# Optimization experiments

Hardware: AMD Instinct MI355X
Metric: run time of the kernel (lower is better)

Reference implementation:

```python
import jax, jax.numpy as jnp
import numpy as np

X_DIM = 512
Y_DIM = 512
HID = 300
N = 2048


def setup_inputs() -> dict:
    key = jax.random.key(0)
    ks = jax.random.split(key, 8)
    scale = 0.05
    return {
        "pos_local": jax.random.normal(ks[0], (N, X_DIM), jnp.float32),
        "pos_global": jax.random.normal(ks[1], (N, Y_DIM), jnp.float32),
        "neg_local": jax.random.normal(ks[2], (N, X_DIM), jnp.float32),
        "neg_global": jax.random.normal(ks[3], (N, Y_DIM), jnp.float32),
        "W1": jax.random.normal(ks[4], (X_DIM + Y_DIM, HID), jnp.float32) * scale,
        "b1": jnp.zeros((HID,), jnp.float32),
        "W2": jax.random.normal(ks[5], (HID, 1), jnp.float32) * scale,
        "b2": jnp.zeros((1,), jnp.float32),
        "batch_size": 256,
    }


def reference(pos_local, pos_global, neg_local, neg_global, W1, b1, W2, b2, batch_size):
    # Split first-layer weight into local/global halves so we never materialize
    # the concatenated pair tensor: F(cat(l, g)) uses l @ W1l + g @ W1g.
    W1l, W1g = W1[:X_DIM], W1[X_DIM:]
    w2, bias2 = W2[:, 0], b2[0]

    # Positive branch: plain batched MLP, chunking does not change the math.
    h0 = jax.nn.relu(pos_local @ W1l + pos_global @ W1g + b1)  # [N, HID]
    t0 = jax.nn.softplus(h0 @ w2 + bias2).mean()

    # Negative branch: per chunk of size B, pair (local_j, global_i),
    # score[i, j] = F(local_j, global_i); logsumexp over j, mean over i.
    nc = neg_local.shape[0] // batch_size
    nl = neg_local.reshape(nc, batch_size, X_DIM)
    ng = neg_global.reshape(nc, batch_size, Y_DIM)

    def chunk_term(carry, lg):
        l, g = lg                                   # [B, x], [B, y]
        lp = l @ W1l                                # [B, HID]
        gp = g @ W1g                                # [B, HID]
        h = jax.nn.relu(gp[:, None, :] + lp[None, :, :] + b1)  # [B, B, HID]
        s = jax.nn.softplus(h @ w2 + bias2)         # [B, B]
        val = jax.scipy.special.logsumexp(s, axis=1).mean()
        return carry + val, None

    total, _ = jax.lax.scan(chunk_term, jnp.float32(0.0), (nl, ng))
    t1 = total / nc

    lower_bound = t0 - t1
    return -lower_bound
```

## Files before the change

### kernel.cpp

```cpp
#include <hip/hip_runtime.h>
#include <math.h>

#define NR   2048
#define XD   512
#define HID  300
#define BS   256
#define NCH  8
#define NPAD 320
#define KTOT 1024
#define GSTR 304
#define NBLK 544

typedef __attribute__((ext_vector_type(8))) short bf16x8;
typedef __attribute__((ext_vector_type(4))) float f32x4;

__device__ __forceinline__ float softplus_f(float x) {
    return fmaxf(x, 0.f) + log1pf(__expf(-fabsf(x)));
}
__device__ __forceinline__ unsigned short f2bf(float f) {
    unsigned int u = __float_as_uint(f);
    u += 0x7FFFu + ((u >> 16) & 1u);
    return (unsigned short)(u >> 16);
}

__global__ __launch_bounds__(256) void convert(
    const float* __restrict__ pl, const float* __restrict__ pg,
    const float* __restrict__ nl, const float* __restrict__ ng,
    const float* __restrict__ W1,
    unsigned short* __restrict__ Aneg, unsigned short* __restrict__ Apos,
    unsigned short* __restrict__ Wt, unsigned int* __restrict__ counter)
{
    const int b = blockIdx.x, tid = threadIdx.x;
    if (b == 0 && tid == 0) *counter = 0u;
    if (b < 4096) {
        const int m = (b < 2048) ? b : b - 2048;
        const float* lo = (b < 2048) ? nl : pl;
        const float* hi = (b < 2048) ? ng : pg;
        unsigned short* dst = (b < 2048) ? Aneg : Apos;
        const int kq = tid * 4;
        const float4 v = (kq < XD) ? *(const float4*)(lo + m * XD + kq)
                                   : *(const float4*)(hi + m * XD + kq - XD);
        ushort4 o;
        o.x = f2bf(v.x); o.y = f2bf(v.y); o.z = f2bf(v.z); o.w = f2bf(v.w);
        *(ushort4*)(dst + m * KTOT + kq) = o;
    } else {
        __shared__ unsigned short ts[16][72];
        const int t = b - 4096;
        const int nt = t % 20, kt = t / 20;
        const int n = nt * 16 + (tid & 15);
        const int kl = tid >> 4;
        #pragma unroll
        for (int j = 0; j < 4; ++j) {
            const int k = kt * 64 + kl * 4 + j;
            const float val = (n < HID) ? W1[k * HID + n] : 0.f;
            ts[tid & 15][kl * 4 + j] = f2bf(val);
        }
        __syncthreads();
        const int nw = tid >> 4, kw = (tid & 15) * 4;
        ushort4 o;
        o.x = ts[nw][kw]; o.y = ts[nw][kw + 1]; o.z = ts[nw][kw + 2]; o.w = ts[nw][kw + 3];
        *(ushort4*)(Wt + (nt * 16 + nw) * KTOT + kt * 64 + kw) = o;
    }
}

__global__ __launch_bounds__(64) void mfma_gemm(
    const unsigned short* __restrict__ Aneg, const unsigned short* __restrict__ Apos,
    const unsigned short* __restrict__ Wt, const float* __restrict__ b1,
    float* __restrict__ LP4, float* __restrict__ GPB,
    float* __restrict__ P0a, float* __restrict__ P0b)
{
    const int job = blockIdx.z;
    const int m0 = blockIdx.x * 32, n0 = blockIdx.y * 32;
    const int lane = threadIdx.x;
    const int r = lane & 15, g = lane >> 4;

    const unsigned short* A = (job >= 2) ? Apos : Aneg;
    const int kbeg = (job & 1) ? XD : 0;

    const unsigned short* a0p = A  + (m0 + r) * KTOT + kbeg + 8 * g;
    const unsigned short* a1p = a0p + 16 * KTOT;
    const unsigned short* b0p = Wt + (n0 + r) * KTOT + kbeg + 8 * g;
    const unsigned short* b1p = b0p + 16 * KTOT;

    f32x4 acc00 = {0,0,0,0}, acc01 = {0,0,0,0}, acc10 = {0,0,0,0}, acc11 = {0,0,0,0};

    #pragma unroll 8
    for (int k = 0; k < XD; k += 32) {
        const bf16x8 a0 = *(const bf16x8*)(a0p + k);
        const bf16x8 a1 = *(const bf16x8*)(a1p + k);
        const bf16x8 w0 = *(const bf16x8*)(b0p + k);
        const bf16x8 w1 = *(const bf16x8*)(b1p + k);
        acc00 = __builtin_amdgcn_mfma_f32_16x16x32_bf16(a0, w0, acc00, 0, 0, 0);
        acc01 = __builtin_amdgcn_mfma_f32_16x16x32_bf16(a0, w1, acc01, 0, 0, 0);
        acc10 = __builtin_amdgcn_mfma_f32_16x16x32_bf16(a1, w0, acc10, 0, 0, 0);
        acc11 = __builtin_amdgcn_mfma_f32_16x16x32_bf16(a1, w1, acc11, 0, 0, 0);
    }

    f32x4 accs[2][2] = {{acc00, acc01}, {acc10, acc11}};
    #pragma unroll
    for (int mi = 0; mi < 2; ++mi) {
        #pragma unroll
        for (int ni = 0; ni < 2; ++ni) {
            const int n = n0 + ni * 16 + r;
            const int mb = m0 + mi * 16 + 4 * g;
            const f32x4 v = accs[mi][ni];
            if (job == 0) {
                float* base = LP4 + ((size_t)(n >> 2) * NR + mb) * 4 + (n & 3);
                base[0] = v[0]; base[4] = v[1]; base[8] = v[2]; base[12] = v[3];
            } else if (n < HID) {
                const float bias = (job == 1) ? b1[n] : 0.f;
                float* out = (job == 1) ? GPB : ((job == 2) ? P0a : P0b);
                #pragma unroll
                for (int j = 0; j < 4; ++j)
                    out[(size_t)(mb + j) * GSTR + n] = v[j] + bias;
            }
        }
    }
}

__global__ __launch_bounds__(256) void fused(
    const float* __restrict__ LP4, const float* __restrict__ GPB,
    const float* __restrict__ P0a, const float* __restrict__ P0b,
    const float* __restrict__ b1, const float* __restrict__ W2,
    const float* __restrict__ b2,
    float* __restrict__ partials, unsigned int* __restrict__ counter,
    float* __restrict__ out)
{
    __shared__ __align__(16) float w2s[HID];
    __shared__ __align__(16) float gbs[4][HID];
    __shared__ float red[4][4];
    __shared__ int sh_last;
    const int tid = threadIdx.x;
    const int bid = blockIdx.x;
    const int wid = tid >> 6;
    float partial = 0.f;

    if (bid < 512) {
        const int chunk = bid >> 6;
        const int g0 = (bid & 63) * 4;
        const float* gp = GPB + (size_t)(chunk * BS + g0) * GSTR;
        for (int idx = tid; idx < HID; idx += 256) {
            w2s[idx] = W2[idx];
            gbs[0][idx] = gp[idx];
            gbs[1][idx] = gp[GSTR + idx];
            gbs[2][idx] = gp[2 * GSTR + idx];
            gbs[3][idx] = gp[3 * GSTR + idx];
        }
        __syncthreads();

        const int lg = chunk * BS + tid;
        const float4* lp4 = (const float4*)LP4 + lg;

        float acc[4] = {0.f, 0.f, 0.f, 0.f};
        float4 a0 = lp4[0];
        float4 a1 = lp4[(size_t)NR];
        for (int k8 = 0; k8 < 37; ++k8) {
            const int k = k8 * 8;
            const float4 n0 = lp4[(size_t)(2 * k8 + 2) * NR];
            const float4 n1 = lp4[(size_t)(2 * k8 + 3) * NR];
            const float4 wa = *(const float4*)&w2s[k];
            const float4 wb = *(const float4*)&w2s[k + 4];
            #pragma unroll
            for (int gt = 0; gt < 4; ++gt) {
                const float4 ga = *(const float4*)&gbs[gt][k];
                const float4 gb = *(const float4*)&gbs[gt][k + 4];
                acc[gt] = fmaf(fmaxf(ga.x + a0.x, 0.f), wa.x, acc[gt]);
                acc[gt] = fmaf(fmaxf(ga.y + a0.y, 0.f), wa.y, acc[gt]);
                acc[gt] = fmaf(fmaxf(ga.z + a0.z, 0.f), wa.z, acc[gt]);
                acc[gt] = fmaf(fmaxf(ga.w + a0.w, 0.f), wa.w, acc[gt]);
                acc[gt] = fmaf(fmaxf(gb.x + a1.x, 0.f), wb.x, acc[gt]);
                acc[gt] = fmaf(fmaxf(gb.y + a1.y, 0.f), wb.y, acc[gt]);
                acc[gt] = fmaf(fmaxf(gb.z + a1.z, 0.f), wb.z, acc[gt]);
                acc[gt] = fmaf(fmaxf(gb.w + a1.w, 0.f), wb.w, acc[gt]);
            }
            a0 = n0; a1 = n1;
        }
        {
            const float4 wt = *(const float4*)&w2s[296];
            #pragma unroll
            for (int gt = 0; gt < 4; ++gt) {
                const float4 ga = *(const float4*)&gbs[gt][296];
                acc[gt] = fmaf(fmaxf(ga.x + a0.x, 0.f), wt.x, acc[gt]);
                acc[gt] = fmaf(fmaxf(ga.y + a0.y, 0.f), wt.y, acc[gt]);
                acc[gt] = fmaf(fmaxf(ga.z + a0.z, 0.f), wt.z, acc[gt]);
                acc[gt] = fmaf(fmaxf(ga.w + a0.w, 0.f), wt.w, acc[gt]);
            }
        }

        const float b2v = b2[0];
        #pragma unroll
        for (int gt = 0; gt < 4; ++gt) {
            float e = __expf(softplus_f(acc[gt] + b2v));
            #pragma unroll
            for (int o = 32; o > 0; o >>= 1) e += __shfl_xor(e, o);
            if ((tid & 63) == 0) red[wid][gt] = e;
        }
        __syncthreads();
        partial = 0.f;
        #pragma unroll
        for (int gt = 0; gt < 4; ++gt)
            partial += __logf(red[0][gt] + red[1][gt] + red[2][gt] + red[3][gt]);
    } else {
        for (int idx = tid; idx < HID; idx += 256) {
            w2s[idx] = W2[idx];
            gbs[0][idx] = b1[idx];
        }
        __syncthreads();
        const int rl = tid >> 2, q = tid & 3;
        const int i = (bid - 512) * 64 + rl;
        const int q0 = q * 19;
        const int q1 = (q == 3) ? HID / 4 : q0 + 19;
        const float4* ra = (const float4*)(P0a + (size_t)i * GSTR);
        const float4* rb = (const float4*)(P0b + (size_t)i * GSTR);
        float acc = 0.f;
        for (int k4 = q0; k4 < q1; ++k4) {
            const float4 a = ra[k4], b = rb[k4];
            const float4 bb = *(const float4*)&gbs[0][k4 * 4];
            const float4 wv = *(const float4*)&w2s[k4 * 4];
            acc += fmaxf(a.x + b.x + bb.x, 0.f) * wv.x
                 + fmaxf(a.y + b.y + bb.y, 0.f) * wv.y
                 + fmaxf(a.z + b.z + bb.z, 0.f) * wv.z
                 + fmaxf(a.w + b.w + bb.w, 0.f) * wv.w;
        }
        acc += __shfl_xor(acc, 1);
        acc += __shfl_xor(acc, 2);
        float sp = (q == 0) ? softplus_f(acc + b2[0]) : 0.f;
        #pragma unroll
        for (int o = 32; o > 0; o >>= 1) sp += __shfl_xor(sp, o);
        if ((tid & 63) == 0) red[wid][0] = sp;
        __syncthreads();
        partial = -(red[0][0] + red[1][0] + red[2][0] + red[3][0]);
    }

    if (tid == 0) {
        partials[bid] = partial;
        __threadfence();
        const unsigned t = atomicAdd(counter, 1u);
        sh_last = (t == NBLK - 1) ? 1 : 0;
    }
    __syncthreads();
    if (sh_last) {
        __threadfence();
        const volatile float* p = (const volatile float*)partials;
        float v = p[tid] + p[tid + 256];
        if (tid + 512 < NBLK) v += p[tid + 512];
        #pragma unroll
        for (int o = 32; o > 0; o >>= 1) v += __shfl_xor(v, o);
        if ((tid & 63) == 0) red[wid][0] = v;
        __syncthreads();
        if (tid == 0)
            out[0] = (red[0][0] + red[1][0] + red[2][0] + red[3][0]) * (1.f / 2048.f);
    }
}

extern "C" void kernel_launch(void* const* d_in, const int* in_sizes, int n_in,
                              void* d_out, int out_size, void* d_ws, size_t ws_size,
                              hipStream_t stream)
{
    const float* pl = (const float*)d_in[0];
    const float* pg = (const float*)d_in[1];
    const float* nl = (const float*)d_in[2];
    const float* ng = (const float*)d_in[3];
    const float* W1 = (const float*)d_in[4];
    const float* b1 = (const float*)d_in[5];
    const float* W2 = (const float*)d_in[6];
    const float* b2 = (const float*)d_in[7];

    char* ws = (char*)d_ws;
    unsigned short* Aneg = (unsigned short*)(ws);
    unsigned short* Apos = (unsigned short*)(ws + (4u << 20));
    unsigned short* Wt   = (unsigned short*)(ws + (8u << 20));
    float* LP4  = (float*)(ws + (9u << 20));
    float* GPB  = (float*)(ws + (12u << 20));
    float* P0a  = (float*)(ws + (15u << 20));
    float* P0b  = (float*)(ws + (18u << 20));
    float* partials = (float*)(ws + (21u << 20));
    unsigned int* counter = (unsigned int*)(ws + (21u << 20) + 4096);
    float* out = (float*)d_out;

    hipLaunchKernelGGL(convert, dim3(4096 + 320), dim3(256), 0, stream,
                       pl, pg, nl, ng, W1, Aneg, Apos, Wt, counter);
    hipLaunchKernelGGL(mfma_gemm, dim3(NR / 32, NPAD / 32, 4), dim3(64), 0, stream,
                       Aneg, Apos, Wt, b1, LP4, GPB, P0a, P0b);
    hipLaunchKernelGGL(fused, dim3(NBLK), dim3(256), 0, stream,
                       LP4, GPB, P0a, P0b, b1, W2, b2, partials, counter, out);
}
```

Baseline: 66.41 us.

## Use relu identity with abs and split pair scoring across more blocks

Rewrites relu(x)*w as 0.5*w*(x+|x|), so the inner loop becomes one abs-FMA per element. The linear part is precomputed once per global row and once per local row. Each negative-chunk unit is split into two blocks over local halves, with the K range split across thread halves and reduced through shared memory. This doubles the block count to fill the GPU better. The exp-sums are written per half and combined with a log in the final last-block reduction. In exchange there is extra shared-memory traffic, more syncs, and a larger final reduction.

```diff
diff --git a/kernel.cpp b/kernel.cpp
--- a/kernel.cpp
+++ b/kernel.cpp
@@ -5,11 +5,10 @@
 #define XD   512
 #define HID  300
 #define BS   256
-#define NCH  8
 #define NPAD 320
 #define KTOT 1024
 #define GSTR 304
-#define NBLK 544
+#define NBLK 1056
 
 typedef __attribute__((ext_vector_type(8))) short bf16x8;
 typedef __attribute__((ext_vector_type(4))) float f32x4;
@@ -52,8 +51,7 @@
         #pragma unroll
         for (int j = 0; j < 4; ++j) {
             const int k = kt * 64 + kl * 4 + j;
-            const float val = (n < HID) ? W1[k * HID + n] : 0.f;
-            ts[tid & 15][kl * 4 + j] = f2bf(val);
+            ts[tid & 15][kl * 4 + j] = f2bf((n < HID) ? W1[k * HID + n] : 0.f);
         }
         __syncthreads();
         const int nw = tid >> 4, kw = (tid & 15) * 4;
@@ -118,29 +116,31 @@
     }
 }
 
-__global__ __launch_bounds__(256) void fused(
+__global__ __launch_bounds__(256, 4) void fused(
     const float* __restrict__ LP4, const float* __restrict__ GPB,
     const float* __restrict__ P0a, const float* __restrict__ P0b,
     const float* __restrict__ b1, const float* __restrict__ W2,
     const float* __restrict__ b2,
-    float* __restrict__ partials, unsigned int* __restrict__ counter,
-    float* __restrict__ out)
+    float* __restrict__ negE, float* __restrict__ posP,
+    unsigned int* __restrict__ counter, float* __restrict__ out)
 {
     __shared__ __align__(16) float w2s[HID];
     __shared__ __align__(16) float gbs[4][HID];
+    __shared__ __align__(16) float pacc[2][128][4];
+    __shared__ float sC[4];
     __shared__ float red[4][4];
     __shared__ int sh_last;
     const int tid = threadIdx.x;
     const int bid = blockIdx.x;
-    const int wid = tid >> 6;
-    float partial = 0.f;
-
-    if (bid < 512) {
-        const int chunk = bid >> 6;
-        const int g0 = (bid & 63) * 4;
+    const int wid = tid >> 6, lane = tid & 63;
+    const float b2v = b2[0];
+
+    if (bid < 1024) {
+        const int unit = bid >> 1, lhalf = bid & 1;
+        const int chunk = unit >> 6, g0 = (unit & 63) * 4;
         const float* gp = GPB + (size_t)(chunk * BS + g0) * GSTR;
         for (int idx = tid; idx < HID; idx += 256) {
-            w2s[idx] = W2[idx];
+            w2s[idx] = 0.5f * W2[idx];
             gbs[0][idx] = gp[idx];
             gbs[1][idx] = gp[GSTR + idx];
             gbs[2][idx] = gp[2 * GSTR + idx];
@@ -148,68 +148,81 @@
         }
         __syncthreads();
 
-        const int lg = chunk * BS + tid;
+        {
+            float c = 0.f;
+            int k4 = lane;
+            if (k4 < 75) {
+                const float4 g4 = *(const float4*)&gbs[wid][k4 * 4];
+                const float4 w4 = *(const float4*)&w2s[k4 * 4];
+                c += g4.x * w4.x + g4.y * w4.y + g4.z * w4.z + g4.w * w4.w;
+            }
+            k4 = lane + 64;
+            if (k4 < 75) {
+                const float4 g4 = *(const float4*)&gbs[wid][k4 * 4];
+                const float4 w4 = *(const float4*)&w2s[k4 * 4];
+                c += g4.x * w4.x + g4.y * w4.y + g4.z * w4.z + g4.w * w4.w;
+            }
+            #pragma unroll
+            for (int o = 32; o > 0; o >>= 1) c += __shfl_xor(c, o);
+            if (lane == 0) sC[wid] = c;
+        }
+
+        const int lh = tid & 127, kh = tid >> 7;
+        const int lg = chunk * BS + lhalf * 128 + lh;
         const float4* lp4 = (const float4*)LP4 + lg;
+        const int k4beg = kh ? 38 : 0;
+        const int k4end = kh ? 75 : 38;
 
         float acc[4] = {0.f, 0.f, 0.f, 0.f};
-        float4 a0 = lp4[0];
-        float4 a1 = lp4[(size_t)NR];
-        for (int k8 = 0; k8 < 37; ++k8) {
-            const int k = k8 * 8;
-            const float4 n0 = lp4[(size_t)(2 * k8 + 2) * NR];
-            const float4 n1 = lp4[(size_t)(2 * k8 + 3) * NR];
-            const float4 wa = *(const float4*)&w2s[k];
-            const float4 wb = *(const float4*)&w2s[k + 4];
+        float q = 0.f;
+        float4 a0 = lp4[(size_t)k4beg * NR];
+        float4 a1 = lp4[(size_t)(k4beg + 1) * NR];
+        for (int k4 = k4beg; k4 < k4end; ++k4) {
+            const float4 nx = lp4[(size_t)(k4 + 2) * NR];
+            const float4 w4 = *(const float4*)&w2s[k4 * 4];
+            q = fmaf(w4.x, a0.x, q); q = fmaf(w4.y, a0.y, q);
+            q = fmaf(w4.z, a0.z, q); q = fmaf(w4.w, a0.w, q);
             #pragma unroll
             for (int gt = 0; gt < 4; ++gt) {
-                const float4 ga = *(const float4*)&gbs[gt][k];
-                const float4 gb = *(const float4*)&gbs[gt][k + 4];
-                acc[gt] = fmaf(fmaxf(ga.x + a0.x, 0.f), wa.x, acc[gt]);
-                acc[gt] = fmaf(fmaxf(ga.y + a0.y, 0.f), wa.y, acc[gt]);
-                acc[gt] = fmaf(fmaxf(ga.z + a0.z, 0.f), wa.z, acc[gt]);
-                acc[gt] = fmaf(fmaxf(ga.w + a0.w, 0.f), wa.w, acc[gt]);
-                acc[gt] = fmaf(fmaxf(gb.x + a1.x, 0.f), wb.x, acc[gt]);
-                acc[gt] = fmaf(fmaxf(gb.y + a1.y, 0.f), wb.y, acc[gt]);
-                acc[gt] = fmaf(fmaxf(gb.z + a1.z, 0.f), wb.z, acc[gt]);
-                acc[gt] = fmaf(fmaxf(gb.w + a1.w, 0.f), wb.w, acc[gt]);
-            }
-            a0 = n0; a1 = n1;
-        }
-        {
-            const float4 wt = *(const float4*)&w2s[296];
+                const float4 g4 = *(const float4*)&gbs[gt][k4 * 4];
+                acc[gt] = fmaf(fabsf(g4.x + a0.x), w4.x, acc[gt]);
+                acc[gt] = fmaf(fabsf(g4.y + a0.y), w4.y, acc[gt]);
+                acc[gt] = fmaf(fabsf(g4.z + a0.z), w4.z, acc[gt]);
+                acc[gt] = fmaf(fabsf(g4.w + a0.w), w4.w, acc[gt]);
+            }
+            a0 = a1; a1 = nx;
+        }
+        __syncthreads();
+        *(float4*)&pacc[kh][lh][0] =
+            make_float4(acc[0] + q, acc[1] + q, acc[2] + q, acc[3] + q);
+        __syncthreads();
+
+        if (tid < 128) {
             #pragma unroll
             for (int gt = 0; gt < 4; ++gt) {
-                const float4 ga = *(const float4*)&gbs[gt][296];
-                acc[gt] = fmaf(fmaxf(ga.x + a0.x, 0.f), wt.x, acc[gt]);
-                acc[gt] = fmaf(fmaxf(ga.y + a0.y, 0.f), wt.y, acc[gt]);
-                acc[gt] = fmaf(fmaxf(ga.z + a0.z, 0.f), wt.z, acc[gt]);
-                acc[gt] = fmaf(fmaxf(ga.w + a0.w, 0.f), wt.w, acc[gt]);
-            }
-        }
-
-        const float b2v = b2[0];
-        #pragma unroll
-        for (int gt = 0; gt < 4; ++gt) {
-            float e = __expf(softplus_f(acc[gt] + b2v));
+                const float s = sC[gt] + pacc[0][lh][gt] + pacc[1][lh][gt];
+                float e = __expf(softplus_f(s + b2v));
+                #pragma unroll
+                for (int o = 32; o > 0; o >>= 1) e += __shfl_xor(e, o);
+                if (lane == 0) red[wid][gt] = e;
+            }
+        }
+        __syncthreads();
+        if (tid == 0) {
             #pragma unroll
-            for (int o = 32; o > 0; o >>= 1) e += __shfl_xor(e, o);
-            if ((tid & 63) == 0) red[wid][gt] = e;
-        }
-        __syncthreads();
-        partial = 0.f;
-        #pragma unroll
-        for (int gt = 0; gt < 4; ++gt)
-            partial += __logf(red[0][gt] + red[1][gt] + red[2][gt] + red[3][gt]);
+            for (int gt = 0; gt < 4; ++gt)
+                negE[unit * 8 + lhalf * 4 + gt] = red[0][gt] + red[1][gt];
+        }
     } else {
         for (int idx = tid; idx < HID; idx += 256) {
             w2s[idx] = W2[idx];
             gbs[0][idx] = b1[idx];
         }
         __syncthreads();
-        const int rl = tid >> 2, q = tid & 3;
-        const int i = (bid - 512) * 64 + rl;
-        const int q0 = q * 19;
-        const int q1 = (q == 3) ? HID / 4 : q0 + 19;
+        const int rl = tid >> 2, qq = tid & 3;
+        const int i = (bid - 1024) * 64 + rl;
+        const int q0 = qq * 19;
+        const int q1 = (qq == 3) ? HID / 4 : q0 + 19;
         const float4* ra = (const float4*)(P0a + (size_t)i * GSTR);
         const float4* rb = (const float4*)(P0b + (size_t)i * GSTR);
         float acc = 0.f;
@@ -224,16 +237,16 @@
         }
         acc += __shfl_xor(acc, 1);
         acc += __shfl_xor(acc, 2);
-        float sp = (q == 0) ? softplus_f(acc + b2[0]) : 0.f;
+        float sp = (qq == 0) ? softplus_f(acc + b2v) : 0.f;
         #pragma unroll
         for (int o = 32; o > 0; o >>= 1) sp += __shfl_xor(sp, o);
         if ((tid & 63) == 0) red[wid][0] = sp;
         __syncthreads();
-        partial = -(red[0][0] + red[1][0] + red[2][0] + red[3][0]);
+        if (tid == 0)
+            posP[bid - 1024] = red[0][0] + red[1][0] + red[2][0] + red[3][0];
     }
 
     if (tid == 0) {
-        partials[bid] = partial;
         __threadfence();
         const unsigned t = atomicAdd(counter, 1u);
         sh_last = (t == NBLK - 1) ? 1 : 0;
@@ -241,12 +254,17 @@
     __syncthreads();
     if (sh_last) {
         __threadfence();
-        const volatile float* p = (const volatile float*)partials;
-        float v = p[tid] + p[tid + 256];
-        if (tid + 512 < NBLK) v += p[tid + 512];
+        const volatile float* ne = (const volatile float*)negE;
+        const volatile float* pp = (const volatile float*)posP;
+        float v = 0.f;
+        for (int i = tid; i < 2048; i += 256) {
+            const int u = i >> 2, gt = i & 3;
+            v += __logf(ne[u * 8 + gt] + ne[u * 8 + 4 + gt]);
+        }
+        if (tid < 32) v -= pp[tid];
         #pragma unroll
         for (int o = 32; o > 0; o >>= 1) v += __shfl_xor(v, o);
-        if ((tid & 63) == 0) red[wid][0] = v;
+        if (lane == 0) red[wid][0] = v;
         __syncthreads();
         if (tid == 0)
             out[0] = (red[0][0] + red[1][0] + red[2][0] + red[3][0]) * (1.f / 2048.f);
@@ -274,14 +292,15 @@
     float* GPB  = (float*)(ws + (12u << 20));
     float* P0a  = (float*)(ws + (15u << 20));
     float* P0b  = (float*)(ws + (18u << 20));
-    float* partials = (float*)(ws + (21u << 20));
-    unsigned int* counter = (unsigned int*)(ws + (21u << 20) + 4096);
-    float* out = (float*)d_out;
+    float* negE = (float*)(ws + (21u << 20));
+    float* posP = negE + 4096;
+    unsigned int* counter = (unsigned int*)(ws + (21u << 20) + 65536);
+    float* out  = (float*)d_out;
 
     hipLaunchKernelGGL(convert, dim3(4096 + 320), dim3(256), 0, stream,
                        pl, pg, nl, ng, W1, Aneg, Apos, Wt, counter);
     hipLaunchKernelGGL(mfma_gemm, dim3(NR / 32, NPAD / 32, 4), dim3(64), 0, stream,
                        Aneg, Apos, Wt, b1, LP4, GPB, P0a, P0b);
     hipLaunchKernelGGL(fused, dim3(NBLK), dim3(256), 0, stream,
-                       LP4, GPB, P0a, P0b, b1, W2, b2, partials, counter, out);
-}
+                       LP4, GPB, P0a, P0b, b1, W2, b2, negE, posP, counter, out);
+}
```

After: 80.68 us. 21.5% more time.
